# Kernel optimization log

Measured on AMD Instinct MI355X. Metric: run time of the kernel, lower is better.

The kernel has to match this reference:

```python
import jax, jax.numpy as jnp
import numpy as np

N, H, W, C = 8, 64, 64, 256
GC = 8            # channels per group (gc)
G = C // GC       # groups = 32
K = 3             # deformable kernel size
KK = K * K
DK = 3            # depthwise kernel size for offset/mask branch


def setup_inputs() -> dict:
    key = jax.random.key(0)
    ks = jax.random.split(key, 6)
    s = 0.02
    return {
        "x": jax.random.normal(ks[0], (N, H, W, C), jnp.float32),
        "dw_w": jax.random.normal(ks[1], (DK, DK, 1, C), jnp.float32) * s,
        "dw_b": jnp.zeros((C,), jnp.float32),
        "om_w": jax.random.normal(ks[2], (C, G * KK * 3), jnp.float32) * s,
        "om_b": jnp.zeros((G * KK * 3,), jnp.float32),
        "vp_w": jax.random.normal(ks[3], (C, C), jnp.float32) * s,
        "vp_b": jnp.zeros((C,), jnp.float32),
        "op_w": jax.random.normal(ks[4], (C, C), jnp.float32) * s,  # output_bias=False
    }


def _dcnv4(x, dw_w, dw_b, om_w, om_b, vp_w, vp_b, op_w):
    n, h, w, c = x.shape
    # --- offset/mask branch: depthwise conv then pointwise linear ---
    xdw = jax.lax.conv_general_dilated(
        x, dw_w, window_strides=(1, 1), padding="SAME",
        dimension_numbers=("NHWC", "HWIO", "NHWC"), feature_group_count=c) + dw_b
    om = (xdw @ om_w + om_b).reshape(n, h, w, G, KK * 3)
    offset = om[..., : 2 * KK].reshape(n, h, w, G, KK, 2)  # (dx, dy) per point
    mask = om[..., 2 * KK :]                                # [n,h,w,G,KK], raw (no softmax in v4)

    # --- value projection ---
    value = (x @ vp_w + vp_b).reshape(n, h, w, G, GC)

    # --- sampling locations: pixel + kernel-grid point + learned offset ---
    kg = (jnp.arange(K) - (K - 1) // 2).astype(jnp.float32)
    ky = jnp.repeat(kg, K)   # [KK]
    kx = jnp.tile(kg, K)     # [KK]
    base_y = jnp.arange(h, dtype=jnp.float32).reshape(1, h, 1, 1, 1)
    base_x = jnp.arange(w, dtype=jnp.float32).reshape(1, 1, w, 1, 1)
    py = base_y + ky + offset[..., 1]  # [n,h,w,G,KK]
    px = base_x + kx + offset[..., 0]

    y0 = jnp.floor(py)
    x0 = jnp.floor(px)
    ty = py - y0
    tx = px - x0

    n_idx = jnp.arange(n).reshape(n, 1, 1, 1, 1)
    g_idx = jnp.arange(G).reshape(1, 1, 1, G, 1)

    def gather(yi, xi):
        valid = (yi >= 0) & (yi <= h - 1) & (xi >= 0) & (xi <= w - 1)
        yc = jnp.clip(yi, 0, h - 1).astype(jnp.int32)
        xc = jnp.clip(xi, 0, w - 1).astype(jnp.int32)
        v = value[n_idx, yc, xc, g_idx]          # [n,h,w,G,KK,GC]
        return v * valid[..., None].astype(value.dtype)

    v00 = gather(y0, x0)
    v01 = gather(y0, x0 + 1)
    v10 = gather(y0 + 1, x0)
    v11 = gather(y0 + 1, x0 + 1)

    sampled = ((1 - ty) * (1 - tx))[..., None] * v00 \
            + ((1 - ty) * tx)[..., None] * v01 \
            + (ty * (1 - tx))[..., None] * v10 \
            + (ty * tx)[..., None] * v11        # [n,h,w,G,KK,GC]

    out = jnp.einsum("nhwgkc,nhwgk->nhwgc", sampled, mask).reshape(n, h, w, c)
    return out @ op_w                            # output proj, no bias


def reference(x, dw_w, dw_b, om_w, om_b, vp_w, vp_b, op_w):
    return _dcnv4(x, dw_w, dw_b, om_w, om_b, vp_w, vp_b, op_w)
```

## Files before the change

kernel.cpp:

```cpp
#include <hip/hip_runtime.h>


typedef __bf16 bf16_t;
typedef bf16_t bf16x8 __attribute__((ext_vector_type(8)));
typedef bf16_t bf16x4 __attribute__((ext_vector_type(4)));
typedef float f32x4 __attribute__((ext_vector_type(4)));

namespace {
constexpr int NN = 8, HH = 64, WW = 64, CC = 256;
constexpr int G = 32, GC = 8, OMD = 864;
constexpr int NPIX = NN * HH * WW;
}

__device__ __forceinline__ size_t fragIdx(int row, int c) {
  return ((size_t)(row >> 4) * 4096) + ((c >> 5) * 512) + (((c >> 3) & 3) * 128) +
         ((row & 15) * 8) + (c & 7);
}

__global__ __launch_bounds__(256) void convert_weights_kernel(
    const float* __restrict__ om_w, const float* __restrict__ vp_w,
    const float* __restrict__ op_w, bf16_t* __restrict__ om_wF,
    bf16_t* __restrict__ vp_wF, bf16_t* __restrict__ op_wF) {
  __shared__ float s_t[64][65];
  const int b = blockIdx.x, t = threadIdx.x;
  const float* src;
  bf16_t* dst;
  int ld, ncols, nt, kt;
  if (b < 56) {
    src = om_w; dst = om_wF; ld = OMD; ncols = OMD; kt = b / 14; nt = b % 14;
  } else if (b < 72) {
    const int i = b - 56;
    src = vp_w; dst = vp_wF; ld = CC; ncols = CC; kt = i >> 2; nt = i & 3;
  } else {
    const int i = b - 72;
    src = op_w; dst = op_wF; ld = CC; ncols = CC; kt = i >> 2; nt = i & 3;
  }
  const int nl = t & 63, kh = t >> 6;
  const int n = nt * 64 + nl;
#pragma unroll
  for (int i = 0; i < 16; ++i) {
    const int kl = kh * 16 + i;
    s_t[kl][nl] = (n < ncols) ? src[(size_t)(kt * 64 + kl) * ld + n] : 0.0f;
  }
  __syncthreads();
  const int lane = t & 63, kq = lane >> 4, n15 = lane & 15, n16 = t >> 6;
#pragma unroll
  for (int it = 0; it < 2; ++it) {
    bf16x8 v;
#pragma unroll
    for (int j = 0; j < 8; ++j) v[j] = (bf16_t)s_t[it * 32 + kq * 8 + j][n16 * 16 + n15];
    const size_t off = (size_t)(nt * 4 + n16) * 4096 + (size_t)(kt * 2 + it) * 512 +
                       kq * 128 + n15 * 8;
    *(bf16x8*)(dst + off) = v;
  }
}

__global__ __launch_bounds__(512, 4) void dwconv_value_kernel(
    const float* __restrict__ x, const float* __restrict__ dw_w,
    const float* __restrict__ dw_b, const bf16_t* __restrict__ vp_wF,
    const float* __restrict__ vp_b, bf16_t* __restrict__ xdwF,
    bf16_t* __restrict__ value_g) {
  __shared__ bf16_t s_xf[64 * 256];

  const int t = threadIdx.x;
  const int row = blockIdx.x;
  const int y = row & 63;
  const int img = row >> 6;

  {
    const int cq = (t & 63) * 4;
    const int seg = t >> 6;
    const bool up = (y > 0), dn = (y < HH - 1);
    const float* xrow = x + (size_t)row * WW * CC + cq;

    const float4 bias = *(const float4*)&dw_b[cq];
    float4 dw[9];
#pragma unroll
    for (int i = 0; i < 9; ++i) dw[i] = *(const float4*)&dw_w[(size_t)i * CC + cq];

    const float4 zero = make_float4(0.f, 0.f, 0.f, 0.f);
    auto loadcol = [&](int xx, float4 c[3]) {
      if (xx < 0 || xx >= WW) { c[0] = c[1] = c[2] = zero; return; }
      c[0] = up ? *(const float4*)(xrow + ((size_t)xx - WW) * CC) : zero;
      c[1] = *(const float4*)(xrow + (size_t)xx * CC);
      c[2] = dn ? *(const float4*)(xrow + ((size_t)xx + WW) * CC) : zero;
    };

    const int x0 = seg * 8;
    float4 cm[3], cc[3], cp[3];
    loadcol(x0 - 1, cm);
    loadcol(x0, cc);

    for (int xx = x0; xx < x0 + 8; ++xx) {
      loadcol(xx + 1, cp);
      float4 a = bias;
#pragma unroll
      for (int r = 0; r < 3; ++r) {
        const float4 w0 = dw[r * 3 + 0], w1 = dw[r * 3 + 1], w2 = dw[r * 3 + 2];
        a.x = fmaf(cm[r].x, w0.x, fmaf(cc[r].x, w1.x, fmaf(cp[r].x, w2.x, a.x)));
        a.y = fmaf(cm[r].y, w0.y, fmaf(cc[r].y, w1.y, fmaf(cp[r].y, w2.y, a.y)));
        a.z = fmaf(cm[r].z, w0.z, fmaf(cc[r].z, w1.z, fmaf(cp[r].z, w2.z, a.z)));
        a.w = fmaf(cm[r].w, w0.w, fmaf(cc[r].w, w1.w, fmaf(cp[r].w, w2.w, a.w)));
      }
      const int pix = row * WW + xx;
      bf16x4 av, cv;
      av[0] = (bf16_t)a.x; av[1] = (bf16_t)a.y; av[2] = (bf16_t)a.z; av[3] = (bf16_t)a.w;
      cv[0] = (bf16_t)cc[1].x; cv[1] = (bf16_t)cc[1].y;
      cv[2] = (bf16_t)cc[1].z; cv[3] = (bf16_t)cc[1].w;
      *(bf16x4*)&xdwF[fragIdx(pix, cq)] = av;
      const int lf = (xx >> 4) * 4096 + ((cq >> 5) * 512) + (((cq >> 3) & 3) * 128) +
                     ((xx & 15) * 8) + (cq & 7);
      *(bf16x4*)&s_xf[lf] = cv;
#pragma unroll
      for (int r = 0; r < 3; ++r) { cm[r] = cc[r]; cc[r] = cp[r]; }
    }
  }
  __syncthreads();

  {
    const int lane = t & 63;
    const int wave = t >> 6;
    const int mq = wave >> 1;
    const int nh = wave & 1;
    const int m = lane & 15;
    const int kq = lane >> 4;

    const bf16_t* Ap = s_xf + mq * 4096 + lane * 8;
    const bf16_t* Bp = vp_wF + (size_t)(nh * 8) * 4096 + lane * 8;

    f32x4 acc[8] = {};
#pragma unroll
    for (int ks = 0; ks < 8; ++ks) {
      const bf16x8 a = *(const bf16x8*)(Ap + ks * 512);
#pragma unroll
      for (int i = 0; i < 8; ++i) {
        const bf16x8 b = *(const bf16x8*)(Bp + (size_t)i * 4096 + ks * 512);
        acc[i] = __builtin_amdgcn_mfma_f32_16x16x32_bf16(a, b, acc[i], 0, 0, 0);
      }
    }

#pragma unroll
    for (int i = 0; i < 8; ++i) {
      const int n = (nh * 8 + i) * 16 + m;
      const float bs = vp_b[n];
      const int g = n >> 3, c = n & 7;
      bf16_t* plane = value_g + ((size_t)(img * G + g) << 15) + c;
#pragma unroll
      for (int r = 0; r < 4; ++r) {
        const int pl = mq * 16 + kq * 4 + r;
        const int pin = y * 64 + pl;
        plane[(size_t)pin * GC] = (bf16_t)(acc[i][r] + bs);
      }
    }
  }
}

__global__ __launch_bounds__(512, 2) void om_gemm_kernel(
    const bf16_t* __restrict__ xdwF, const bf16_t* __restrict__ om_wF,
    const float* __restrict__ om_b, bf16_t* __restrict__ omP) {
  __shared__ bf16_t s_a[64 * 256];

  const int t = threadIdx.x;
  const int lane = t & 63;
  const int wave = t >> 6;

  {
    const bf16_t* src = xdwF + (size_t)blockIdx.x * 16384;
#pragma unroll
    for (int i = 0; i < 4; ++i) {
      const int idx = (i * 512 + t) * 8;
      *(bf16x8*)(s_a + idx) = *(const bf16x8*)(src + idx);
    }
  }
  __syncthreads();

  const int m = lane & 15;
  const int kq = lane >> 4;
  const bf16_t* Bp = om_wF + (size_t)(wave * 7) * 4096 + lane * 8;

  f32x4 acc[4][7] = {};
#pragma unroll
  for (int ks = 0; ks < 8; ++ks) {
    bf16x8 a[4];
#pragma unroll
    for (int mt = 0; mt < 4; ++mt)
      a[mt] = *(const bf16x8*)(s_a + mt * 4096 + ks * 512 + lane * 8);
#pragma unroll
    for (int i = 0; i < 7; ++i) {
      const bf16x8 b = *(const bf16x8*)(Bp + (size_t)i * 4096 + ks * 512);
#pragma unroll
      for (int mt = 0; mt < 4; ++mt)
        acc[mt][i] =
            __builtin_amdgcn_mfma_f32_16x16x32_bf16(a[mt], b, acc[mt][i], 0, 0, 0);
    }
  }

  const int pix0 = blockIdx.x * 64;
  const int img = pix0 >> 12;
  const int pin0 = pix0 & 4095;
#pragma unroll
  for (int i = 0; i < 7; ++i) {
    const int nt = wave * 7 + i;
    if (nt < 54) {
      const int n = nt * 16 + m;
      const float bs = om_b[n];
      const int g = n / 27;
      const int j = n - g * 27;
      bf16_t* dst = omP + ((size_t)(img * G + g) * 4096 + pin0) * 32 + j;
#pragma unroll
      for (int mt = 0; mt < 4; ++mt)
#pragma unroll
        for (int r = 0; r < 4; ++r) {
          const int pl = mt * 16 + kq * 4 + r;
          dst[(size_t)pl * 32] = (bf16_t)(acc[mt][i][r] + bs);
        }
    }
  }
}

__global__ __launch_bounds__(512, 2) void sample_kernel(
    const bf16_t* __restrict__ omP, const bf16_t* __restrict__ value_g,
    bf16_t* __restrict__ sampledF) {
  __shared__ bf16x8 s_v[66 * 66];

  const int t = threadIdx.x;
  const int b = blockIdx.x;
  const int img = b >> 6;
  const int g = (b >> 1) & 31;
  const int half = b & 1;

  {
    const bf16x8 zv = {};
    for (int i = t; i < 260; i += 512) {
      int Y, X;
      if (i < 66)       { Y = 0;            X = i; }
      else if (i < 132) { Y = 65;           X = i - 66; }
      else if (i < 196) { Y = i - 132 + 1;  X = 0; }
      else              { Y = i - 196 + 1;  X = 65; }
      s_v[Y * 66 + X] = zv;
    }
    const bf16x8* plane = (const bf16x8*)(value_g + ((size_t)(img * G + g) << 15));
#pragma unroll
    for (int i = 0; i < 8; ++i) {
      const int c = i * 512 + t;
      const int yy = c >> 6, xx = c & 63;
      s_v[(yy + 1) * 66 + (xx + 1)] = plane[c];
    }
  }
  __syncthreads();

  const bf16_t* omBase =
      omP + ((size_t)(img * G + g) * 4096 + (size_t)half * 2048) * 32;

#pragma unroll
  for (int it = 0; it < 4; ++it) {
    const int pl = it * 512 + t;
    const int px = half * 2048 + pl;
    const int xw = px & 63;
    const int y = px >> 6;

    const bf16_t* op = omBase + (size_t)pl * 32;
    const bf16x8 o0 = *(const bf16x8*)(op + 0);
    const bf16x8 o1 = *(const bf16x8*)(op + 8);
    const bf16x8 o2 = *(const bf16x8*)(op + 16);
    const bf16x8 o3 = *(const bf16x8*)(op + 24);
    float arr[27];
#pragma unroll
    for (int j = 0; j < 8; ++j) {
      arr[j] = (float)o0[j];
      arr[8 + j] = (float)o1[j];
      arr[16 + j] = (float)o2[j];
    }
#pragma unroll
    for (int j = 0; j < 3; ++j) arr[24 + j] = (float)o3[j];

    float acc[GC];
#pragma unroll
    for (int c = 0; c < GC; ++c) acc[c] = 0.0f;

#pragma unroll
    for (int k = 0; k < 9; ++k) {
      const float pxf = (float)(xw + (k % 3) - 1) + arr[2 * k];
      const float pyf = (float)(y + (k / 3) - 1) + arr[2 * k + 1];
      const float mk = arr[18 + k];
      const float x0f = floorf(pxf), y0f = floorf(pyf);
      const float tx = pxf - x0f, ty = pyf - y0f;
      const int ix = (int)x0f, iy = (int)y0f;

      const int iX0 = min(max(ix, -1), 64) + 1;
      const int iX1 = min(max(ix + 1, -1), 64) + 1;
      const int iY0 = min(max(iy, -1), 64) + 1;
      const int iY1 = min(max(iy + 1, -1), 64) + 1;

      const bf16x8 v00 = s_v[iY0 * 66 + iX0];
      const bf16x8 v01 = s_v[iY0 * 66 + iX1];
      const bf16x8 v10 = s_v[iY1 * 66 + iX0];
      const bf16x8 v11 = s_v[iY1 * 66 + iX1];

      const float w00 = mk * (1.0f - ty) * (1.0f - tx);
      const float w01 = mk * (1.0f - ty) * tx;
      const float w10 = mk * ty * (1.0f - tx);
      const float w11 = mk * ty * tx;

#pragma unroll
      for (int c = 0; c < GC; ++c) {
        float s = acc[c];
        s = fmaf(w00, (float)v00[c], s);
        s = fmaf(w01, (float)v01[c], s);
        s = fmaf(w10, (float)v10[c], s);
        s = fmaf(w11, (float)v11[c], s);
        acc[c] = s;
      }
    }

    bf16x8 sv;
#pragma unroll
    for (int c = 0; c < GC; ++c) sv[c] = (bf16_t)acc[c];
    *(bf16x8*)(sampledF + fragIdx(img * 4096 + px, g * 8)) = sv;
  }
}

__global__ __launch_bounds__(512, 4) void out_gemm_kernel(
    const bf16_t* __restrict__ AF, const bf16_t* __restrict__ BF,
    float* __restrict__ out) {
  const int lane = threadIdx.x & 63;
  const int wave = threadIdx.x >> 6;
  const int mq = wave >> 1;
  const int nh = wave & 1;
  const int mt = blockIdx.x * 4 + mq;
  const int m = lane & 15;
  const int kq = lane >> 4;

  const bf16_t* Ap = AF + (size_t)mt * 4096 + lane * 8;
  const bf16_t* Bp = BF + (size_t)(nh * 8) * 4096 + lane * 8;

  f32x4 acc[8] = {};
#pragma unroll
  for (int ks = 0; ks < 8; ++ks) {
    const bf16x8 a = *(const bf16x8*)(Ap + ks * 512);
#pragma unroll
    for (int i = 0; i < 8; ++i) {
      const bf16x8 b = *(const bf16x8*)(Bp + (size_t)i * 4096 + ks * 512);
      acc[i] = __builtin_amdgcn_mfma_f32_16x16x32_bf16(a, b, acc[i], 0, 0, 0);
    }
  }

#pragma unroll
  for (int i = 0; i < 8; ++i) {
    const int n = (nh * 8 + i) * 16 + m;
#pragma unroll
    for (int r = 0; r < 4; ++r) {
      const int pix = mt * 16 + kq * 4 + r;
      out[(size_t)pix * CC + n] = acc[i][r];
    }
  }
}

extern "C" void kernel_launch(void* const* d_in, const int* in_sizes, int n_in,
                              void* d_out, int out_size, void* d_ws, size_t ws_size,
                              hipStream_t stream) {
  const float* x = (const float*)d_in[0];
  const float* dw_w = (const float*)d_in[1];
  const float* dw_b = (const float*)d_in[2];
  const float* om_w = (const float*)d_in[3];
  const float* om_b = (const float*)d_in[4];
  const float* vp_w = (const float*)d_in[5];
  const float* vp_b = (const float*)d_in[6];
  const float* op_w = (const float*)d_in[7];
  float* out = (float*)d_out;

  char* ws = (char*)d_ws;
  bf16_t* omP = (bf16_t*)ws;
  bf16_t* value_g = (bf16_t*)(ws + 67108864);
  bf16_t* xdwF = (bf16_t*)(ws + 83886080);
  bf16_t* sampledF = xdwF;
  bf16_t* om_wF = (bf16_t*)(ws + 100663296);
  bf16_t* vp_wF = (bf16_t*)(ws + 101122048);
  bf16_t* op_wF = (bf16_t*)(ws + 101253120);

  convert_weights_kernel<<<88, 256, 0, stream>>>(om_w, vp_w, op_w,
                                                 om_wF, vp_wF, op_wF);
  dwconv_value_kernel<<<NN * HH, 512, 0, stream>>>(x, dw_w, dw_b, vp_wF, vp_b,
                                                   xdwF, value_g);
  om_gemm_kernel<<<NPIX / 64, 512, 0, stream>>>(xdwF, om_wF, om_b, omP);
  sample_kernel<<<NPIX / 64, 512, 0, stream>>>(omP, value_g, sampledF);
  out_gemm_kernel<<<NPIX / 64, 512, 0, stream>>>(sampledF, op_wF, out);
}
```

Measured before the change: 230.3 us.

## Fuse offset/mask GEMM into sampling kernel with per-group weight layout

```diff
diff --git a/kernel.cpp b/kernel.cpp
--- a/kernel.cpp
+++ b/kernel.cpp
@@ -8,7 +8,7 @@
 
 namespace {
 constexpr int NN = 8, HH = 64, WW = 64, CC = 256;
-constexpr int G = 32, GC = 8, OMD = 864;
+constexpr int G = 32, GC = 8;
 constexpr int NPIX = NN * HH * WW;
 }
 
@@ -19,39 +19,55 @@
 
 __global__ __launch_bounds__(256) void convert_weights_kernel(
     const float* __restrict__ om_w, const float* __restrict__ vp_w,
-    const float* __restrict__ op_w, bf16_t* __restrict__ om_wF,
+    const float* __restrict__ op_w, bf16_t* __restrict__ om_wG,
     bf16_t* __restrict__ vp_wF, bf16_t* __restrict__ op_wF) {
   __shared__ float s_t[64][65];
+  __shared__ float s_w[256][27];
   const int b = blockIdx.x, t = threadIdx.x;
-  const float* src;
-  bf16_t* dst;
-  int ld, ncols, nt, kt;
-  if (b < 56) {
-    src = om_w; dst = om_wF; ld = OMD; ncols = OMD; kt = b / 14; nt = b % 14;
-  } else if (b < 72) {
-    const int i = b - 56;
-    src = vp_w; dst = vp_wF; ld = CC; ncols = CC; kt = i >> 2; nt = i & 3;
+  if (b < 32) {
+    const float* src;
+    bf16_t* dst;
+    int kt, nt;
+    if (b < 16) { src = vp_w; dst = vp_wF; kt = b >> 2; nt = b & 3; }
+    else        { src = op_w; dst = op_wF; kt = (b - 16) >> 2; nt = (b - 16) & 3; }
+    const int nl = t & 63, kh = t >> 6;
+    const int n = nt * 64 + nl;
+#pragma unroll
+    for (int i = 0; i < 16; ++i) {
+      const int kl = kh * 16 + i;
+      s_t[kl][nl] = src[(size_t)(kt * 64 + kl) * CC + n];
+    }
+    __syncthreads();
+    const int lane = t & 63, kq = lane >> 4, n15 = lane & 15, n16 = t >> 6;
+#pragma unroll
+    for (int it = 0; it < 2; ++it) {
+      bf16x8 v;
+#pragma unroll
+      for (int j = 0; j < 8; ++j)
+        v[j] = (bf16_t)s_t[it * 32 + kq * 8 + j][n16 * 16 + n15];
+      const size_t off = (size_t)(nt * 4 + n16) * 4096 + (size_t)(kt * 2 + it) * 512 +
+                         kq * 128 + n15 * 8;
+      *(bf16x8*)(dst + off) = v;
+    }
   } else {
-    const int i = b - 72;
-    src = op_w; dst = op_wF; ld = CC; ncols = CC; kt = i >> 2; nt = i & 3;
-  }
-  const int nl = t & 63, kh = t >> 6;
-  const int n = nt * 64 + nl;
-#pragma unroll
-  for (int i = 0; i < 16; ++i) {
-    const int kl = kh * 16 + i;
-    s_t[kl][nl] = (n < ncols) ? src[(size_t)(kt * 64 + kl) * ld + n] : 0.0f;
-  }
-  __syncthreads();
-  const int lane = t & 63, kq = lane >> 4, n15 = lane & 15, n16 = t >> 6;
-#pragma unroll
-  for (int it = 0; it < 2; ++it) {
-    bf16x8 v;
-#pragma unroll
-    for (int j = 0; j < 8; ++j) v[j] = (bf16_t)s_t[it * 32 + kq * 8 + j][n16 * 16 + n15];
-    const size_t off = (size_t)(nt * 4 + n16) * 4096 + (size_t)(kt * 2 + it) * 512 +
-                       kq * 128 + n15 * 8;
-    *(bf16x8*)(dst + off) = v;
+    const int g = b - 32;
+#pragma unroll
+    for (int j = 0; j < 27; ++j) s_w[t][j] = om_w[(size_t)t * 864 + g * 27 + j];
+    __syncthreads();
+#pragma unroll
+    for (int i = 0; i < 4; ++i) {
+      const int chunk = i * 256 + t;
+      const int tile = chunk >> 9, ks = (chunk >> 6) & 7, kq = (chunk >> 4) & 3,
+                n15 = chunk & 15;
+      const int j = tile * 16 + n15;
+      bf16x8 v;
+#pragma unroll
+      for (int cl = 0; cl < 8; ++cl) {
+        const int c = ks * 32 + kq * 8 + cl;
+        v[cl] = (j < 27) ? (bf16_t)s_w[c][j] : (bf16_t)0.0f;
+      }
+      *(bf16x8*)(om_wG + ((size_t)g << 13) + (size_t)chunk * 8) = v;
+    }
   }
 }
 
@@ -155,124 +171,94 @@
   }
 }
 
-__global__ __launch_bounds__(512, 2) void om_gemm_kernel(
-    const bf16_t* __restrict__ xdwF, const bf16_t* __restrict__ om_wF,
-    const float* __restrict__ om_b, bf16_t* __restrict__ omP) {
-  __shared__ bf16_t s_a[64 * 256];
-
-  const int t = threadIdx.x;
-  const int lane = t & 63;
-  const int wave = t >> 6;
-
-  {
-    const bf16_t* src = xdwF + (size_t)blockIdx.x * 16384;
-#pragma unroll
-    for (int i = 0; i < 4; ++i) {
-      const int idx = (i * 512 + t) * 8;
-      *(bf16x8*)(s_a + idx) = *(const bf16x8*)(src + idx);
-    }
-  }
-  __syncthreads();
-
-  const int m = lane & 15;
-  const int kq = lane >> 4;
-  const bf16_t* Bp = om_wF + (size_t)(wave * 7) * 4096 + lane * 8;
-
-  f32x4 acc[4][7] = {};
-#pragma unroll
-  for (int ks = 0; ks < 8; ++ks) {
-    bf16x8 a[4];
-#pragma unroll
-    for (int mt = 0; mt < 4; ++mt)
-      a[mt] = *(const bf16x8*)(s_a + mt * 4096 + ks * 512 + lane * 8);
-#pragma unroll
-    for (int i = 0; i < 7; ++i) {
-      const bf16x8 b = *(const bf16x8*)(Bp + (size_t)i * 4096 + ks * 512);
-#pragma unroll
-      for (int mt = 0; mt < 4; ++mt)
-        acc[mt][i] =
-            __builtin_amdgcn_mfma_f32_16x16x32_bf16(a[mt], b, acc[mt][i], 0, 0, 0);
-    }
-  }
-
-  const int pix0 = blockIdx.x * 64;
-  const int img = pix0 >> 12;
-  const int pin0 = pix0 & 4095;
-#pragma unroll
-  for (int i = 0; i < 7; ++i) {
-    const int nt = wave * 7 + i;
-    if (nt < 54) {
-      const int n = nt * 16 + m;
-      const float bs = om_b[n];
-      const int g = n / 27;
-      const int j = n - g * 27;
-      bf16_t* dst = omP + ((size_t)(img * G + g) * 4096 + pin0) * 32 + j;
-#pragma unroll
-      for (int mt = 0; mt < 4; ++mt)
-#pragma unroll
-        for (int r = 0; r < 4; ++r) {
-          const int pl = mt * 16 + kq * 4 + r;
-          dst[(size_t)pl * 32] = (bf16_t)(acc[mt][i][r] + bs);
-        }
-    }
-  }
-}
-
-__global__ __launch_bounds__(512, 2) void sample_kernel(
-    const bf16_t* __restrict__ omP, const bf16_t* __restrict__ value_g,
+__global__ __launch_bounds__(512, 2) void oms_kernel(
+    const bf16_t* __restrict__ xdwF, const bf16_t* __restrict__ om_wG,
+    const float* __restrict__ om_b, const bf16_t* __restrict__ value_g,
     bf16_t* __restrict__ sampledF) {
   __shared__ bf16x8 s_v[66 * 66];
+  __shared__ float s_om[8][64][32];
 
   const int t = threadIdx.x;
+  const int lane = t & 63, wave = t >> 6;
   const int b = blockIdx.x;
-  const int img = b >> 6;
-  const int g = (b >> 1) & 31;
-  const int half = b & 1;
+  const int img = b & 7, g = (b >> 3) & 31, quarter = b >> 8;
+  const int c15 = lane & 15, kq = lane >> 4;
+  const int tile0 = img * 256 + quarter * 64;
+
+  bf16x8 wf[2][8];
+  {
+    const bf16_t* base = om_wG + ((size_t)g << 13) + (size_t)lane * 8;
+#pragma unroll
+    for (int n2 = 0; n2 < 2; ++n2)
+#pragma unroll
+      for (int ks = 0; ks < 8; ++ks)
+        wf[n2][ks] = *(const bf16x8*)(base + n2 * 4096 + ks * 512);
+  }
+  float bias[2][4];
+#pragma unroll
+  for (int n2 = 0; n2 < 2; ++n2)
+#pragma unroll
+    for (int r = 0; r < 4; ++r) {
+      const int j = n2 * 16 + kq * 4 + r;
+      bias[n2][r] = (j < 27) ? om_b[g * 27 + j] : 0.0f;
+    }
 
   {
     const bf16x8 zv = {};
     for (int i = t; i < 260; i += 512) {
       int Y, X;
-      if (i < 66)       { Y = 0;            X = i; }
-      else if (i < 132) { Y = 65;           X = i - 66; }
-      else if (i < 196) { Y = i - 132 + 1;  X = 0; }
-      else              { Y = i - 196 + 1;  X = 65; }
+      if (i < 66)       { Y = 0;           X = i; }
+      else if (i < 132) { Y = 65;          X = i - 66; }
+      else if (i < 196) { Y = i - 132 + 1; X = 0; }
+      else              { Y = i - 196 + 1; X = 65; }
       s_v[Y * 66 + X] = zv;
     }
     const bf16x8* plane = (const bf16x8*)(value_g + ((size_t)(img * G + g) << 15));
 #pragma unroll
     for (int i = 0; i < 8; ++i) {
       const int c = i * 512 + t;
-      const int yy = c >> 6, xx = c & 63;
-      s_v[(yy + 1) * 66 + (xx + 1)] = plane[c];
-    }
-  }
-  __syncthreads();
-
-  const bf16_t* omBase =
-      omP + ((size_t)(img * G + g) * 4096 + (size_t)half * 2048) * 32;
-
-#pragma unroll
-  for (int it = 0; it < 4; ++it) {
-    const int pl = it * 512 + t;
-    const int px = half * 2048 + pl;
-    const int xw = px & 63;
-    const int y = px >> 6;
-
-    const bf16_t* op = omBase + (size_t)pl * 32;
-    const bf16x8 o0 = *(const bf16x8*)(op + 0);
-    const bf16x8 o1 = *(const bf16x8*)(op + 8);
-    const bf16x8 o2 = *(const bf16x8*)(op + 16);
-    const bf16x8 o3 = *(const bf16x8*)(op + 24);
-    float arr[27];
-#pragma unroll
-    for (int j = 0; j < 8; ++j) {
-      arr[j] = (float)o0[j];
-      arr[8 + j] = (float)o1[j];
-      arr[16 + j] = (float)o2[j];
-    }
-#pragma unroll
-    for (int j = 0; j < 3; ++j) arr[24 + j] = (float)o3[j];
+      s_v[((c >> 6) + 1) * 66 + (c & 63) + 1] = plane[c];
+    }
+  }
+
+  auto do_mfma = [&](const int grp) {
+    const int tb = tile0 + wave * 8 + grp * 4;
+#pragma unroll
+    for (int q = 0; q < 4; ++q) {
+      const bf16_t* Ap = xdwF + ((size_t)(tb + q)) * 4096 + (size_t)lane * 8;
+      f32x4 a0 = {}, a1 = {};
+#pragma unroll
+      for (int ks = 0; ks < 8; ++ks) {
+        const bf16x8 xf = *(const bf16x8*)(Ap + ks * 512);
+        a0 = __builtin_amdgcn_mfma_f32_16x16x32_bf16(wf[0][ks], xf, a0, 0, 0, 0);
+        a1 = __builtin_amdgcn_mfma_f32_16x16x32_bf16(wf[1][ks], xf, a1, 0, 0, 0);
+      }
+      const int p = q * 16 + c15;
+      const int key = p & 7;
+      f32x4 v0, v1;
+#pragma unroll
+      for (int r = 0; r < 4; ++r) {
+        v0[r] = a0[r] + bias[0][r];
+        v1[r] = a1[r] + bias[1][r];
+      }
+      float* row = &s_om[wave][p][0];
+      *(f32x4*)(row + ((kq ^ key) << 2)) = v0;
+      *(f32x4*)(row + (((4 + kq) ^ key) << 2)) = v1;
+    }
+  };
+
+  auto do_sample = [&](const int grp) {
+    const int pin = quarter * 1024 + wave * 128 + grp * 64 + lane;
+    const float* row = &s_om[wave][lane][0];
+    const int key = lane & 7;
+    float arr[28];
+#pragma unroll
+    for (int s8 = 0; s8 < 7; ++s8) {
+      const f32x4 v = *(const f32x4*)(row + ((s8 ^ key) << 2));
+      arr[s8 * 4 + 0] = v[0]; arr[s8 * 4 + 1] = v[1];
+      arr[s8 * 4 + 2] = v[2]; arr[s8 * 4 + 3] = v[3];
+    }
+    const int xw = pin & 63, y = pin >> 6;
 
     float acc[GC];
 #pragma unroll
@@ -316,8 +302,14 @@
     bf16x8 sv;
 #pragma unroll
     for (int c = 0; c < GC; ++c) sv[c] = (bf16_t)acc[c];
-    *(bf16x8*)(sampledF + fragIdx(img * 4096 + px, g * 8)) = sv;
-  }
+    *(bf16x8*)(sampledF + fragIdx(img * 4096 + pin, g * 8)) = sv;
+  };
+
+  do_mfma(0);
+  __syncthreads();
+  do_sample(0);
+  do_mfma(1);
+  do_sample(1);
 }
 
 __global__ __launch_bounds__(512, 4) void out_gemm_kernel(
@@ -370,19 +362,17 @@
   float* out = (float*)d_out;
 
   char* ws = (char*)d_ws;
-  bf16_t* omP = (bf16_t*)ws;
-  bf16_t* value_g = (bf16_t*)(ws + 67108864);
-  bf16_t* xdwF = (bf16_t*)(ws + 83886080);
-  bf16_t* sampledF = xdwF;
-  bf16_t* om_wF = (bf16_t*)(ws + 100663296);
-  bf16_t* vp_wF = (bf16_t*)(ws + 101122048);
-  bf16_t* op_wF = (bf16_t*)(ws + 101253120);
-
-  convert_weights_kernel<<<88, 256, 0, stream>>>(om_w, vp_w, op_w,
-                                                 om_wF, vp_wF, op_wF);
+  bf16_t* value_g = (bf16_t*)ws;
+  bf16_t* xdwF = (bf16_t*)(ws + 16777216);
+  bf16_t* sampledF = (bf16_t*)(ws + 33554432);
+  bf16_t* om_wG = (bf16_t*)(ws + 50331648);
+  bf16_t* vp_wF = (bf16_t*)(ws + 50855936);
+  bf16_t* op_wF = (bf16_t*)(ws + 50987008);
+
+  convert_weights_kernel<<<64, 256, 0, stream>>>(om_w, vp_w, op_w,
+                                                 om_wG, vp_wF, op_wF);
   dwconv_value_kernel<<<NN * HH, 512, 0, stream>>>(x, dw_w, dw_b, vp_wF, vp_b,
                                                    xdwF, value_g);
-  om_gemm_kernel<<<NPIX / 64, 512, 0, stream>>>(xdwF, om_wF, om_b, omP);
-  sample_kernel<<<NPIX / 64, 512, 0, stream>>>(omP, value_g, sampledF);
+  oms_kernel<<<1024, 512, 0, stream>>>(xdwF, om_wG, om_b, value_g, sampledF);
   out_gemm_kernel<<<NPIX / 64, 512, 0, stream>>>(sampledF, op_wF, out);
 }
```

Measured after the change: 205.9 us. -10.6%, faster.
